# Kernel tuning notes

Measured on AMD Instinct MI355X. Metric: run time of the kernel, lower is better.

Reference implementation:

```python
import jax, jax.numpy as jnp
import numpy as np

D_IN = 1024
D_OUT = 1024
SEQ = 4096


def setup_inputs() -> dict:
    key = jax.random.key(0)
    k0, k1, k2, k3 = jax.random.split(key, 4)
    inputs = jax.random.normal(k0, (SEQ, D_IN), dtype=jnp.float32)
    # original uses torch.rand (uniform [0,1)) for weights
    W_q = jax.random.uniform(k1, (D_IN, D_OUT), dtype=jnp.float32)
    W_k = jax.random.uniform(k2, (D_IN, D_OUT), dtype=jnp.float32)
    W_v = jax.random.uniform(k3, (D_IN, D_OUT), dtype=jnp.float32)
    return {"inputs": inputs, "W_q": W_q, "W_k": W_k, "W_v": W_v}


def reference(inputs, W_q, W_k, W_v):
    queries = inputs @ W_q            # [S, d_out]
    keys = inputs @ W_k               # [S, d_out]
    values = inputs @ W_v             # [S, d_out]
    d_k = keys.shape[-1]
    scale = 1.0 / jnp.sqrt(jnp.asarray(d_k, dtype=queries.dtype))
    attn_scores = queries @ keys.T    # [S, S]
    attn_weights = jax.nn.softmax(attn_scores * scale, axis=-1)
    context_vectors = attn_weights @ values  # [S, d_out]
    return context_vectors
```

## Files before the change

kernel.cpp:

```cpp
#include <hip/hip_runtime.h>

typedef unsigned short u16;
typedef __attribute__((ext_vector_type(8))) short bf16x8;
typedef __attribute__((ext_vector_type(4))) float f32x4;

#define SEQ 4096
#define DIM 1024

__device__ __forceinline__ u16 f2bf(float f) {
  unsigned u = __float_as_uint(f);
  return (u16)((u + 0x7fffu + ((u >> 16) & 1u)) >> 16);
}
__device__ __forceinline__ float bf2f(u16 h) {
  return __uint_as_float(((unsigned)h) << 16);
}

__device__ __forceinline__ void gload_lds16(const void* g, void* l) {
  __builtin_amdgcn_global_load_lds(
      (const __attribute__((address_space(1))) void*)g,
      (__attribute__((address_space(3))) void*)l, 16, 0, 0);
}

__device__ __forceinline__ size_t pkoff(int row, int col, int kd) {
  int tile = (row >> 7) * (kd >> 5) + (col >> 5);
  int r7 = row & 127, c5 = col & 31;
  int slot = ((r7 >> 4) << 6) | ((c5 >> 3) << 4) | (r7 & 15);
  return (size_t)tile * 4096 + (size_t)(slot * 8 + (c5 & 7));
}

__device__ __forceinline__ void stage_tile_pk(const u16* __restrict__ g,
                                              u16* lds, int tid) {
  const int w = tid >> 6;
  gload_lds16(g + (size_t)tid * 8, lds + (size_t)(w * 64) * 8);
  gload_lds16(g + (size_t)(256 + tid) * 8, lds + (size_t)(256 + w * 64) * 8);
}

template <int NPAIR>
__device__ __forceinline__ void gemm_multi_pk(
    const u16* A0, const u16* A1, const u16* B0, const u16* B1,
    int nkb, u16* lds, f32x4 (&acc)[4][4]) {
  const int tid = threadIdx.x;
  const int w = tid >> 6, l = tid & 63;
  const int wm = w >> 1, wn = w & 1;
  u16* lA0 = lds;
  u16* lB0 = lds + 4096;
  u16* lA1 = lds + 8192;
  u16* lB1 = lds + 12288;

#pragma unroll
  for (int mi = 0; mi < 4; ++mi)
#pragma unroll
    for (int ni = 0; ni < 4; ++ni)
      acc[mi][ni] = (f32x4){0.f, 0.f, 0.f, 0.f};

  const int ao = wm * 2048 + l * 8;
  const int bo = wn * 2048 + l * 8;

  for (int kb = 0; kb < nkb; ++kb) {
    stage_tile_pk(A0 + (size_t)kb * 4096, lA0, tid);
    stage_tile_pk(B0 + (size_t)kb * 4096, lB0, tid);
    if constexpr (NPAIR >= 3) {
      stage_tile_pk(A1 + (size_t)kb * 4096, lA1, tid);
      stage_tile_pk(B1 + (size_t)kb * 4096, lB1, tid);
    }
    __syncthreads();
    bf16x8 a0[4], b0[4];
#pragma unroll
    for (int i = 0; i < 4; ++i) {
      a0[i] = *(const bf16x8*)(lA0 + ao + i * 512);
      b0[i] = *(const bf16x8*)(lB0 + bo + i * 512);
    }
#pragma unroll
    for (int mi = 0; mi < 4; ++mi)
#pragma unroll
      for (int ni = 0; ni < 4; ++ni)
        acc[mi][ni] = __builtin_amdgcn_mfma_f32_16x16x32_bf16(
            a0[mi], b0[ni], acc[mi][ni], 0, 0, 0);
    if constexpr (NPAIR >= 3) {
      bf16x8 b1[4];
#pragma unroll
      for (int i = 0; i < 4; ++i) b1[i] = *(const bf16x8*)(lB1 + bo + i * 512);
#pragma unroll
      for (int mi = 0; mi < 4; ++mi)
#pragma unroll
        for (int ni = 0; ni < 4; ++ni)
          acc[mi][ni] = __builtin_amdgcn_mfma_f32_16x16x32_bf16(
              a0[mi], b1[ni], acc[mi][ni], 0, 0, 0);
      bf16x8 a1[4];
#pragma unroll
      for (int i = 0; i < 4; ++i) a1[i] = *(const bf16x8*)(lA1 + ao + i * 512);
#pragma unroll
      for (int mi = 0; mi < 4; ++mi)
#pragma unroll
        for (int ni = 0; ni < 4; ++ni)
          acc[mi][ni] = __builtin_amdgcn_mfma_f32_16x16x32_bf16(
              a1[mi], b0[ni], acc[mi][ni], 0, 0, 0);
    }
    __syncthreads();
  }
}

__device__ __forceinline__ void gemm_one64(
    const u16* A, const u16* B, int nkb, u16* lds, f32x4 (&acc)[4][4]) {
  const int tid = threadIdx.x;
  const int w = tid >> 6, l = tid & 63;
  const int wm = w >> 1, wn = w & 1;
  u16* lA = lds;
  u16* lB = lds + 8192;

#pragma unroll
  for (int mi = 0; mi < 4; ++mi)
#pragma unroll
    for (int ni = 0; ni < 4; ++ni)
      acc[mi][ni] = (f32x4){0.f, 0.f, 0.f, 0.f};

  const int ao = wm * 2048 + l * 8;
  const int bo = wn * 2048 + l * 8;

  for (int kb = 0; kb < nkb; kb += 2) {
    stage_tile_pk(A + (size_t)kb * 4096, lA, tid);
    stage_tile_pk(A + (size_t)(kb + 1) * 4096, lA + 4096, tid);
    stage_tile_pk(B + (size_t)kb * 4096, lB, tid);
    stage_tile_pk(B + (size_t)(kb + 1) * 4096, lB + 4096, tid);
    __syncthreads();
#pragma unroll
    for (int h = 0; h < 2; ++h) {
      bf16x8 av[4], bv[4];
#pragma unroll
      for (int i = 0; i < 4; ++i) {
        av[i] = *(const bf16x8*)(lA + h * 4096 + ao + i * 512);
        bv[i] = *(const bf16x8*)(lB + h * 4096 + bo + i * 512);
      }
#pragma unroll
      for (int mi = 0; mi < 4; ++mi)
#pragma unroll
        for (int ni = 0; ni < 4; ++ni)
          acc[mi][ni] = __builtin_amdgcn_mfma_f32_16x16x32_bf16(
              av[mi], bv[ni], acc[mi][ni], 0, 0, 0);
    }
    __syncthreads();
  }
}

#define EPILOGUE_IDX                                          \
  const int tid = threadIdx.x, w = tid >> 6, l = tid & 63;    \
  const int wm = w >> 1, wn = w & 1, lr = l & 15, q = l >> 4; \
  (void)tid;


__global__ __launch_bounds__(256) void prep_kernel(
    const float* __restrict__ X,
    const float* __restrict__ W0, const float* __restrict__ W1, const float* __restrict__ W2,
    u16* __restrict__ Xh, u16* __restrict__ Xl,
    u16* __restrict__ H0, u16* __restrict__ L0,
    u16* __restrict__ H1, u16* __restrict__ L1,
    u16* __restrict__ H2) {
  const int z = blockIdx.z;
  const int tx = threadIdx.x, ty = threadIdx.y;
  if (z == 0) {
    int idx = (blockIdx.y * 32 + blockIdx.x) * 256 + ty * 32 + tx;
    int row = idx >> 6;
    int c0 = (idx & 63) * 16;
    u16 h[16], lo[16];
#pragma unroll
    for (int j = 0; j < 4; ++j) {
      float4 x = *(const float4*)(X + (size_t)row * DIM + c0 + j * 4);
      float v;
      v = x.x; h[j*4+0] = f2bf(v); lo[j*4+0] = f2bf(v - bf2f(h[j*4+0]));
      v = x.y; h[j*4+1] = f2bf(v); lo[j*4+1] = f2bf(v - bf2f(h[j*4+1]));
      v = x.z; h[j*4+2] = f2bf(v); lo[j*4+2] = f2bf(v - bf2f(h[j*4+2]));
      v = x.w; h[j*4+3] = f2bf(v); lo[j*4+3] = f2bf(v - bf2f(h[j*4+3]));
    }
    size_t o0 = pkoff(row, c0, DIM);
    size_t o1 = pkoff(row, c0 + 8, DIM);
#pragma unroll
    for (int j = 0; j < 2; ++j) {
      *(ushort4*)(Xh + o0 + j * 4) = *(ushort4*)(h + j * 4);
      *(ushort4*)(Xl + o0 + j * 4) = *(ushort4*)(lo + j * 4);
      *(ushort4*)(Xh + o1 + j * 4) = *(ushort4*)(h + 8 + j * 4);
      *(ushort4*)(Xl + o1 + j * 4) = *(ushort4*)(lo + 8 + j * 4);
    }
    return;
  }
  __shared__ float t[32][33];
  const float* W = (z == 1) ? W0 : (z == 2) ? W1 : W2;
  u16* H = (z == 1) ? H0 : (z == 2) ? H1 : H2;
  u16* L = (z == 1) ? L0 : (z == 2) ? L1 : nullptr;
  const int i0 = blockIdx.y * 32, o0 = blockIdx.x * 32;
#pragma unroll
  for (int m = 0; m < 4; ++m)
    t[ty + 8 * m][tx] = W[(size_t)(i0 + ty + 8 * m) * DIM + o0 + tx];
  __syncthreads();
#pragma unroll
  for (int m = 0; m < 4; ++m) {
    float v = t[tx][ty + 8 * m];
    u16 h = f2bf(v);
    size_t o = pkoff(o0 + ty + 8 * m, i0 + tx, DIM);
    H[o] = h;
    if (L) L[o] = f2bf(v - bf2f(h));
  }
}

__global__ __launch_bounds__(256) void qkv_kernel(
    const u16* __restrict__ Xh, const u16* __restrict__ Xl,
    const u16* __restrict__ Wh0, const u16* __restrict__ Wl0,
    const u16* __restrict__ Wh1, const u16* __restrict__ Wl1,
    const u16* __restrict__ Wh2,
    u16* __restrict__ Qh, u16* __restrict__ Ql,
    u16* __restrict__ Kh, u16* __restrict__ Kl,
    u16* __restrict__ VT) {
  __shared__ __align__(16) u16 lds[4 * 4096];
  const int z = blockIdx.z;
  f32x4 acc[4][4];
  if (z < 2) {
    const u16* Wh = z ? Wh1 : Wh0;
    const u16* Wl = z ? Wl1 : Wl0;
    const int row0 = blockIdx.y * 128, col0 = blockIdx.x * 128;
    gemm_multi_pk<3>(Xh + (size_t)row0 * DIM, Xl + (size_t)row0 * DIM,
                     Wh + (size_t)col0 * DIM, Wl + (size_t)col0 * DIM,
                     DIM / 32, lds, acc);
    EPILOGUE_IDX
    u16* H = z ? Kh : Qh;
    u16* L = z ? Kl : Ql;
#pragma unroll
    for (int mi = 0; mi < 4; ++mi)
#pragma unroll
      for (int ni = 0; ni < 4; ++ni)
#pragma unroll
        for (int r = 0; r < 4; ++r) {
          int row = row0 + wm * 64 + mi * 16 + q * 4 + r;
          int col = col0 + wn * 64 + ni * 16 + lr;
          float v = acc[mi][ni][r];
          u16 h = f2bf(v);
          size_t o = pkoff(row, col, DIM);
          H[o] = h;
          L[o] = f2bf(v - bf2f(h));
        }
  } else {
    const int row0 = blockIdx.x * 128;
    const int col0 = blockIdx.y * 128;
    gemm_one64(Wh2 + (size_t)row0 * DIM, Xh + (size_t)col0 * DIM,
               DIM / 32, lds, acc);
    EPILOGUE_IDX
#pragma unroll
    for (int mi = 0; mi < 4; ++mi)
#pragma unroll
      for (int ni = 0; ni < 4; ++ni)
#pragma unroll
        for (int r = 0; r < 4; ++r) {
          int row = row0 + wm * 64 + mi * 16 + q * 4 + r;
          int col = col0 + wn * 64 + ni * 16 + lr;
          VT[pkoff(row, col, SEQ)] = f2bf(acc[mi][ni][r]);
        }
  }
}

__global__ __launch_bounds__(256) void s_kernel(
    const u16* __restrict__ Qh, const u16* __restrict__ Ql,
    const u16* __restrict__ Kh, const u16* __restrict__ Kl,
    float* __restrict__ S) {
  __shared__ __align__(16) u16 lds[4 * 4096];
  const int row0 = blockIdx.y * 128, col0 = blockIdx.x * 128;
  f32x4 acc[4][4];
  gemm_multi_pk<3>(Qh + (size_t)row0 * DIM, Ql + (size_t)row0 * DIM,
                   Kh + (size_t)col0 * DIM, Kl + (size_t)col0 * DIM,
                   DIM / 32, lds, acc);
  EPILOGUE_IDX
  const float scale = 0.03125f;
#pragma unroll
  for (int mi = 0; mi < 4; ++mi)
#pragma unroll
    for (int ni = 0; ni < 4; ++ni)
#pragma unroll
      for (int r = 0; r < 4; ++r) {
        int row = row0 + wm * 64 + mi * 16 + q * 4 + r;
        int col = col0 + wn * 64 + ni * 16 + lr;
        S[(size_t)row * SEQ + col] = acc[mi][ni][r] * scale;
      }
}

__global__ __launch_bounds__(256) void softmax_kernel(const float* __restrict__ S,
                                                      u16* __restrict__ P) {
  const int row = blockIdx.x;
  const float* s = S + (size_t)row * SEQ;
  const int tid = threadIdx.x;
  float v[16];
  float mx = -3.4e38f;
#pragma unroll
  for (int i = 0; i < 16; ++i) {
    v[i] = s[tid + i * 256];
    mx = fmaxf(mx, v[i]);
  }
#pragma unroll
  for (int off = 32; off; off >>= 1) mx = fmaxf(mx, __shfl_xor(mx, off));
  __shared__ float red[8];
  const int w = tid >> 6, l = tid & 63;
  if (l == 0) red[w] = mx;
  __syncthreads();
  mx = fmaxf(fmaxf(red[0], red[1]), fmaxf(red[2], red[3]));
  float sum = 0.f;
#pragma unroll
  for (int i = 0; i < 16; ++i) {
    v[i] = __expf(v[i] - mx);
    sum += v[i];
  }
#pragma unroll
  for (int off = 32; off; off >>= 1) sum += __shfl_xor(sum, off);
  if (l == 0) red[4 + w] = sum;
  __syncthreads();
  sum = red[4] + red[5] + red[6] + red[7];
  const float inv = 1.f / sum;
#pragma unroll
  for (int i = 0; i < 16; ++i)
    P[pkoff(row, tid + i * 256, SEQ)] = f2bf(v[i] * inv);
}

__global__ __launch_bounds__(256) void o_kernel(const u16* __restrict__ P,
                                                const u16* __restrict__ VT,
                                                float* __restrict__ Opart) {
  __shared__ __align__(16) u16 lds[4 * 4096];
  const int z = blockIdx.z;
  const int row0 = blockIdx.y * 128, col0 = blockIdx.x * 128;
  const u16* A = P + (size_t)row0 * SEQ + (size_t)z * 32 * 4096;
  const u16* B = VT + (size_t)col0 * SEQ + (size_t)z * 32 * 4096;
  f32x4 acc[4][4];
  gemm_one64(A, B, 32, lds, acc);
  EPILOGUE_IDX
  float* O = Opart + (size_t)z * SEQ * DIM;
#pragma unroll
  for (int mi = 0; mi < 4; ++mi)
#pragma unroll
    for (int ni = 0; ni < 4; ++ni)
#pragma unroll
      for (int r = 0; r < 4; ++r) {
        int row = row0 + wm * 64 + mi * 16 + q * 4 + r;
        int col = col0 + wn * 64 + ni * 16 + lr;
        O[(size_t)row * DIM + col] = acc[mi][ni][r];
      }
}

__global__ __launch_bounds__(256) void o_reduce_kernel(const float* __restrict__ Op,
                                                       float* __restrict__ O) {
  const size_t N = (size_t)SEQ * DIM;
  size_t i = ((size_t)blockIdx.x * 256 + threadIdx.x) * 4;
  float4 a = *(const float4*)(Op + i);
  float4 b = *(const float4*)(Op + N + i);
  float4 c = *(const float4*)(Op + 2 * N + i);
  float4 d = *(const float4*)(Op + 3 * N + i);
  float4 r;
  r.x = (a.x + b.x) + (c.x + d.x);
  r.y = (a.y + b.y) + (c.y + d.y);
  r.z = (a.z + b.z) + (c.z + d.z);
  r.w = (a.w + b.w) + (c.w + d.w);
  *(float4*)(O + i) = r;
}

extern "C" void kernel_launch(void* const* d_in, const int* in_sizes, int n_in,
                              void* d_out, int out_size, void* d_ws, size_t ws_size,
                              hipStream_t stream) {
  const float* X = (const float*)d_in[0];
  const float* Wq = (const float*)d_in[1];
  const float* Wk = (const float*)d_in[2];
  const float* Wv = (const float*)d_in[3];

  const size_t MB = 1024 * 1024;
  char* w = (char*)d_ws;
  u16* Xh = (u16*)(w + 0 * MB);
  u16* Xl = (u16*)(w + 8 * MB);
  u16* WqhT = (u16*)(w + 16 * MB);
  u16* WqlT = (u16*)(w + 18 * MB);
  u16* WkhT = (u16*)(w + 20 * MB);
  u16* WklT = (u16*)(w + 22 * MB);
  u16* WvhT = (u16*)(w + 24 * MB);
  u16* Qh = (u16*)(w + 26 * MB);
  u16* Ql = (u16*)(w + 34 * MB);
  u16* Kh = (u16*)(w + 42 * MB);
  u16* Kl = (u16*)(w + 50 * MB);
  u16* VT = (u16*)(w + 58 * MB);
  float* S = (float*)(w + 66 * MB);
  u16* P = (u16*)(w + 26 * MB);
  float* Opart = (float*)(w + 66 * MB);

  prep_kernel<<<dim3(32, 32, 4), dim3(32, 8), 0, stream>>>(
      X, Wq, Wk, Wv, Xh, Xl, WqhT, WqlT, WkhT, WklT, WvhT);
  qkv_kernel<<<dim3(DIM / 128, SEQ / 128, 3), 256, 0, stream>>>(
      Xh, Xl, WqhT, WqlT, WkhT, WklT, WvhT, Qh, Ql, Kh, Kl, VT);
  s_kernel<<<dim3(SEQ / 128, SEQ / 128), 256, 0, stream>>>(Qh, Ql, Kh, Kl, S);
  softmax_kernel<<<SEQ, 256, 0, stream>>>(S, P);
  o_kernel<<<dim3(DIM / 128, SEQ / 128, 4), 256, 0, stream>>>(P, VT, Opart);
  o_reduce_kernel<<<(SEQ * DIM) / (256 * 4), 256, 0, stream>>>(Opart, (float*)d_out);
}
```

Measured before the change: 340.6 us.

## Switch GEMMs to 32x32x16 MFMA and vectorize prep/softmax stores

Replaces the 16x16x32 bf16 MFMA tiling (4x4 accumulators per wave) with 32x32x16 MFMA (2x2 f32x16 accumulators) in all GEMM helpers. The LDS fragment addressing and the epilogue row/column mapping are reworked for the new accumulator layout. The aim is fewer MFMA issues and fewer LDS fragment reads per K step. It also changes softmax to contiguous float4 loads and 16-byte packed stores of P, and packs the prep kernel's X stores into 16-byte writes. The risk is a wrong fragment-to-packed-layout mapping, and the epilogue's global writes become less coalesced.

```diff
diff --git a/kernel.cpp b/kernel.cpp
--- a/kernel.cpp
+++ b/kernel.cpp
@@ -2,7 +2,7 @@
 
 typedef unsigned short u16;
 typedef __attribute__((ext_vector_type(8))) short bf16x8;
-typedef __attribute__((ext_vector_type(4))) float f32x4;
+typedef __attribute__((ext_vector_type(16))) float f32x16;
 
 #define SEQ 4096
 #define DIM 1024
@@ -35,26 +35,30 @@
   gload_lds16(g + (size_t)(256 + tid) * 8, lds + (size_t)(256 + w * 64) * 8);
 }
 
+#define MFMA32(a, b, c) __builtin_amdgcn_mfma_f32_32x32x16_bf16((a), (b), (c), 0, 0, 0)
+
 template <int NPAIR>
 __device__ __forceinline__ void gemm_multi_pk(
     const u16* A0, const u16* A1, const u16* B0, const u16* B1,
-    int nkb, u16* lds, f32x4 (&acc)[4][4]) {
+    int nkb, u16* lds, f32x16 (&acc)[2][2]) {
   const int tid = threadIdx.x;
   const int w = tid >> 6, l = tid & 63;
   const int wm = w >> 1, wn = w & 1;
+  const int lbase = ((l & 31) >> 4) * 512 + (l >> 5) * 128 + (l & 15) * 8;
   u16* lA0 = lds;
   u16* lB0 = lds + 4096;
   u16* lA1 = lds + 8192;
   u16* lB1 = lds + 12288;
 
 #pragma unroll
-  for (int mi = 0; mi < 4; ++mi)
-#pragma unroll
-    for (int ni = 0; ni < 4; ++ni)
-      acc[mi][ni] = (f32x4){0.f, 0.f, 0.f, 0.f};
-
-  const int ao = wm * 2048 + l * 8;
-  const int bo = wn * 2048 + l * 8;
+  for (int ms = 0; ms < 2; ++ms)
+#pragma unroll
+    for (int ns = 0; ns < 2; ++ns)
+#pragma unroll
+      for (int i = 0; i < 16; ++i) acc[ms][ns][i] = 0.f;
+
+  const int ao = wm * 2048 + lbase;
+  const int bo = wn * 2048 + lbase;
 
   for (int kb = 0; kb < nkb; ++kb) {
     stage_tile_pk(A0 + (size_t)kb * 4096, lA0, tid);
@@ -64,58 +68,71 @@
       stage_tile_pk(B1 + (size_t)kb * 4096, lB1, tid);
     }
     __syncthreads();
-    bf16x8 a0[4], b0[4];
-#pragma unroll
-    for (int i = 0; i < 4; ++i) {
-      a0[i] = *(const bf16x8*)(lA0 + ao + i * 512);
-      b0[i] = *(const bf16x8*)(lB0 + bo + i * 512);
-    }
-#pragma unroll
-    for (int mi = 0; mi < 4; ++mi)
-#pragma unroll
-      for (int ni = 0; ni < 4; ++ni)
-        acc[mi][ni] = __builtin_amdgcn_mfma_f32_16x16x32_bf16(
-            a0[mi], b0[ni], acc[mi][ni], 0, 0, 0);
+    bf16x8 a0[2][2], b0[2][2];
+#pragma unroll
+    for (int ms = 0; ms < 2; ++ms)
+#pragma unroll
+      for (int ks = 0; ks < 2; ++ks) {
+        a0[ms][ks] = *(const bf16x8*)(lA0 + ao + ms * 1024 + ks * 256);
+        b0[ms][ks] = *(const bf16x8*)(lB0 + bo + ms * 1024 + ks * 256);
+      }
+#pragma unroll
+    for (int ms = 0; ms < 2; ++ms)
+#pragma unroll
+      for (int ns = 0; ns < 2; ++ns)
+#pragma unroll
+        for (int ks = 0; ks < 2; ++ks)
+          acc[ms][ns] = MFMA32(a0[ms][ks], b0[ns][ks], acc[ms][ns]);
     if constexpr (NPAIR >= 3) {
-      bf16x8 b1[4];
-#pragma unroll
-      for (int i = 0; i < 4; ++i) b1[i] = *(const bf16x8*)(lB1 + bo + i * 512);
-#pragma unroll
-      for (int mi = 0; mi < 4; ++mi)
-#pragma unroll
-        for (int ni = 0; ni < 4; ++ni)
-          acc[mi][ni] = __builtin_amdgcn_mfma_f32_16x16x32_bf16(
-              a0[mi], b1[ni], acc[mi][ni], 0, 0, 0);
-      bf16x8 a1[4];
-#pragma unroll
-      for (int i = 0; i < 4; ++i) a1[i] = *(const bf16x8*)(lA1 + ao + i * 512);
-#pragma unroll
-      for (int mi = 0; mi < 4; ++mi)
-#pragma unroll
-        for (int ni = 0; ni < 4; ++ni)
-          acc[mi][ni] = __builtin_amdgcn_mfma_f32_16x16x32_bf16(
-              a1[mi], b0[ni], acc[mi][ni], 0, 0, 0);
+      bf16x8 b1[2][2];
+#pragma unroll
+      for (int ns = 0; ns < 2; ++ns)
+#pragma unroll
+        for (int ks = 0; ks < 2; ++ks)
+          b1[ns][ks] = *(const bf16x8*)(lB1 + bo + ns * 1024 + ks * 256);
+#pragma unroll
+      for (int ms = 0; ms < 2; ++ms)
+#pragma unroll
+        for (int ns = 0; ns < 2; ++ns)
+#pragma unroll
+          for (int ks = 0; ks < 2; ++ks)
+            acc[ms][ns] = MFMA32(a0[ms][ks], b1[ns][ks], acc[ms][ns]);
+      bf16x8 a1[2][2];
+#pragma unroll
+      for (int ms = 0; ms < 2; ++ms)
+#pragma unroll
+        for (int ks = 0; ks < 2; ++ks)
+          a1[ms][ks] = *(const bf16x8*)(lA1 + ao + ms * 1024 + ks * 256);
+#pragma unroll
+      for (int ms = 0; ms < 2; ++ms)
+#pragma unroll
+        for (int ns = 0; ns < 2; ++ns)
+#pragma unroll
+          for (int ks = 0; ks < 2; ++ks)
+            acc[ms][ns] = MFMA32(a1[ms][ks], b0[ns][ks], acc[ms][ns]);
     }
     __syncthreads();
   }
 }
 
 __device__ __forceinline__ void gemm_one64(
-    const u16* A, const u16* B, int nkb, u16* lds, f32x4 (&acc)[4][4]) {
+    const u16* A, const u16* B, int nkb, u16* lds, f32x16 (&acc)[2][2]) {
   const int tid = threadIdx.x;
   const int w = tid >> 6, l = tid & 63;
   const int wm = w >> 1, wn = w & 1;
+  const int lbase = ((l & 31) >> 4) * 512 + (l >> 5) * 128 + (l & 15) * 8;
   u16* lA = lds;
   u16* lB = lds + 8192;
 
 #pragma unroll
-  for (int mi = 0; mi < 4; ++mi)
-#pragma unroll
-    for (int ni = 0; ni < 4; ++ni)
-      acc[mi][ni] = (f32x4){0.f, 0.f, 0.f, 0.f};
-
-  const int ao = wm * 2048 + l * 8;
-  const int bo = wn * 2048 + l * 8;
+  for (int ms = 0; ms < 2; ++ms)
+#pragma unroll
+    for (int ns = 0; ns < 2; ++ns)
+#pragma unroll
+      for (int i = 0; i < 16; ++i) acc[ms][ns][i] = 0.f;
+
+  const int ao = wm * 2048 + lbase;
+  const int bo = wn * 2048 + lbase;
 
   for (int kb = 0; kb < nkb; kb += 2) {
     stage_tile_pk(A + (size_t)kb * 4096, lA, tid);
@@ -124,28 +141,30 @@
     stage_tile_pk(B + (size_t)(kb + 1) * 4096, lB + 4096, tid);
     __syncthreads();
 #pragma unroll
-    for (int h = 0; h < 2; ++h) {
-      bf16x8 av[4], bv[4];
-#pragma unroll
-      for (int i = 0; i < 4; ++i) {
-        av[i] = *(const bf16x8*)(lA + h * 4096 + ao + i * 512);
-        bv[i] = *(const bf16x8*)(lB + h * 4096 + bo + i * 512);
-      }
-#pragma unroll
-      for (int mi = 0; mi < 4; ++mi)
-#pragma unroll
-        for (int ni = 0; ni < 4; ++ni)
-          acc[mi][ni] = __builtin_amdgcn_mfma_f32_16x16x32_bf16(
-              av[mi], bv[ni], acc[mi][ni], 0, 0, 0);
+    for (int ht = 0; ht < 2; ++ht) {
+      bf16x8 av[2][2], bv[2][2];
+#pragma unroll
+      for (int ms = 0; ms < 2; ++ms)
+#pragma unroll
+        for (int ks = 0; ks < 2; ++ks) {
+          av[ms][ks] = *(const bf16x8*)(lA + ht * 4096 + ao + ms * 1024 + ks * 256);
+          bv[ms][ks] = *(const bf16x8*)(lB + ht * 4096 + bo + ms * 1024 + ks * 256);
+        }
+#pragma unroll
+      for (int ms = 0; ms < 2; ++ms)
+#pragma unroll
+        for (int ns = 0; ns < 2; ++ns)
+#pragma unroll
+          for (int ks = 0; ks < 2; ++ks)
+            acc[ms][ns] = MFMA32(av[ms][ks], bv[ns][ks], acc[ms][ns]);
     }
     __syncthreads();
   }
 }
 
-#define EPILOGUE_IDX                                          \
-  const int tid = threadIdx.x, w = tid >> 6, l = tid & 63;    \
-  const int wm = w >> 1, wn = w & 1, lr = l & 15, q = l >> 4; \
-  (void)tid;
+#define EPILOGUE_IDX32                                     \
+  const int tid = threadIdx.x, w = tid >> 6, l = tid & 63; \
+  const int wm = w >> 1, wn = w & 1, r = l & 31, h = l >> 5; (void)tid;
 
 
 __global__ __launch_bounds__(256) void prep_kernel(
@@ -161,25 +180,27 @@
     int idx = (blockIdx.y * 32 + blockIdx.x) * 256 + ty * 32 + tx;
     int row = idx >> 6;
     int c0 = (idx & 63) * 16;
-    u16 h[16], lo[16];
+    bf16x8 h0, h1, l0v, l1v;
 #pragma unroll
     for (int j = 0; j < 4; ++j) {
       float4 x = *(const float4*)(X + (size_t)row * DIM + c0 + j * 4);
+      u16 hh, ll;
       float v;
-      v = x.x; h[j*4+0] = f2bf(v); lo[j*4+0] = f2bf(v - bf2f(h[j*4+0]));
-      v = x.y; h[j*4+1] = f2bf(v); lo[j*4+1] = f2bf(v - bf2f(h[j*4+1]));
-      v = x.z; h[j*4+2] = f2bf(v); lo[j*4+2] = f2bf(v - bf2f(h[j*4+2]));
-      v = x.w; h[j*4+3] = f2bf(v); lo[j*4+3] = f2bf(v - bf2f(h[j*4+3]));
+      v = x.x; hh = f2bf(v); ll = f2bf(v - bf2f(hh));
+      if (j < 2) { h0[j*4+0] = (short)hh; l0v[j*4+0] = (short)ll; } else { h1[(j-2)*4+0] = (short)hh; l1v[(j-2)*4+0] = (short)ll; }
+      v = x.y; hh = f2bf(v); ll = f2bf(v - bf2f(hh));
+      if (j < 2) { h0[j*4+1] = (short)hh; l0v[j*4+1] = (short)ll; } else { h1[(j-2)*4+1] = (short)hh; l1v[(j-2)*4+1] = (short)ll; }
+      v = x.z; hh = f2bf(v); ll = f2bf(v - bf2f(hh));
+      if (j < 2) { h0[j*4+2] = (short)hh; l0v[j*4+2] = (short)ll; } else { h1[(j-2)*4+2] = (short)hh; l1v[(j-2)*4+2] = (short)ll; }
+      v = x.w; hh = f2bf(v); ll = f2bf(v - bf2f(hh));
+      if (j < 2) { h0[j*4+3] = (short)hh; l0v[j*4+3] = (short)ll; } else { h1[(j-2)*4+3] = (short)hh; l1v[(j-2)*4+3] = (short)ll; }
     }
     size_t o0 = pkoff(row, c0, DIM);
     size_t o1 = pkoff(row, c0 + 8, DIM);
-#pragma unroll
-    for (int j = 0; j < 2; ++j) {
-      *(ushort4*)(Xh + o0 + j * 4) = *(ushort4*)(h + j * 4);
-      *(ushort4*)(Xl + o0 + j * 4) = *(ushort4*)(lo + j * 4);
-      *(ushort4*)(Xh + o1 + j * 4) = *(ushort4*)(h + 8 + j * 4);
-      *(ushort4*)(Xl + o1 + j * 4) = *(ushort4*)(lo + 8 + j * 4);
-    }
+    *(bf16x8*)(Xh + o0) = h0;
+    *(bf16x8*)(Xl + o0) = l0v;
+    *(bf16x8*)(Xh + o1) = h1;
+    *(bf16x8*)(Xl + o1) = l1v;
     return;
   }
   __shared__ float t[32][33];
@@ -211,7 +232,7 @@
     u16* __restrict__ VT) {
   __shared__ __align__(16) u16 lds[4 * 4096];
   const int z = blockIdx.z;
-  f32x4 acc[4][4];
+  f32x16 acc[2][2];
   if (z < 2) {
     const u16* Wh = z ? Wh1 : Wh0;
     const u16* Wl = z ? Wl1 : Wl0;
@@ -219,38 +240,38 @@
     gemm_multi_pk<3>(Xh + (size_t)row0 * DIM, Xl + (size_t)row0 * DIM,
                      Wh + (size_t)col0 * DIM, Wl + (size_t)col0 * DIM,
                      DIM / 32, lds, acc);
-    EPILOGUE_IDX
+    EPILOGUE_IDX32
     u16* H = z ? Kh : Qh;
     u16* L = z ? Kl : Ql;
 #pragma unroll
-    for (int mi = 0; mi < 4; ++mi)
-#pragma unroll
-      for (int ni = 0; ni < 4; ++ni)
-#pragma unroll
-        for (int r = 0; r < 4; ++r) {
-          int row = row0 + wm * 64 + mi * 16 + q * 4 + r;
-          int col = col0 + wn * 64 + ni * 16 + lr;
-          float v = acc[mi][ni][r];
-          u16 h = f2bf(v);
+    for (int ms = 0; ms < 2; ++ms)
+#pragma unroll
+      for (int ns = 0; ns < 2; ++ns)
+#pragma unroll
+        for (int reg = 0; reg < 16; ++reg) {
+          int row = row0 + wm * 64 + ms * 32 + (reg & 3) + 8 * (reg >> 2) + 4 * h;
+          int col = col0 + wn * 64 + ns * 32 + r;
+          float v = acc[ms][ns][reg];
+          u16 hh = f2bf(v);
           size_t o = pkoff(row, col, DIM);
-          H[o] = h;
-          L[o] = f2bf(v - bf2f(h));
+          H[o] = hh;
+          L[o] = f2bf(v - bf2f(hh));
         }
   } else {
     const int row0 = blockIdx.x * 128;
     const int col0 = blockIdx.y * 128;
     gemm_one64(Wh2 + (size_t)row0 * DIM, Xh + (size_t)col0 * DIM,
                DIM / 32, lds, acc);
-    EPILOGUE_IDX
-#pragma unroll
-    for (int mi = 0; mi < 4; ++mi)
-#pragma unroll
-      for (int ni = 0; ni < 4; ++ni)
-#pragma unroll
-        for (int r = 0; r < 4; ++r) {
-          int row = row0 + wm * 64 + mi * 16 + q * 4 + r;
-          int col = col0 + wn * 64 + ni * 16 + lr;
-          VT[pkoff(row, col, SEQ)] = f2bf(acc[mi][ni][r]);
+    EPILOGUE_IDX32
+#pragma unroll
+    for (int ms = 0; ms < 2; ++ms)
+#pragma unroll
+      for (int ns = 0; ns < 2; ++ns)
+#pragma unroll
+        for (int reg = 0; reg < 16; ++reg) {
+          int row = row0 + wm * 64 + ms * 32 + (reg & 3) + 8 * (reg >> 2) + 4 * h;
+          int col = col0 + wn * 64 + ns * 32 + r;
+          VT[pkoff(row, col, SEQ)] = f2bf(acc[ms][ns][reg]);
         }
   }
 }
@@ -261,21 +282,21 @@
     float* __restrict__ S) {
   __shared__ __align__(16) u16 lds[4 * 4096];
   const int row0 = blockIdx.y * 128, col0 = blockIdx.x * 128;
-  f32x4 acc[4][4];
+  f32x16 acc[2][2];
   gemm_multi_pk<3>(Qh + (size_t)row0 * DIM, Ql + (size_t)row0 * DIM,
                    Kh + (size_t)col0 * DIM, Kl + (size_t)col0 * DIM,
                    DIM / 32, lds, acc);
-  EPILOGUE_IDX
+  EPILOGUE_IDX32
   const float scale = 0.03125f;
 #pragma unroll
-  for (int mi = 0; mi < 4; ++mi)
-#pragma unroll
-    for (int ni = 0; ni < 4; ++ni)
-#pragma unroll
-      for (int r = 0; r < 4; ++r) {
-        int row = row0 + wm * 64 + mi * 16 + q * 4 + r;
-        int col = col0 + wn * 64 + ni * 16 + lr;
-        S[(size_t)row * SEQ + col] = acc[mi][ni][r] * scale;
+  for (int ms = 0; ms < 2; ++ms)
+#pragma unroll
+    for (int ns = 0; ns < 2; ++ns)
+#pragma unroll
+      for (int reg = 0; reg < 16; ++reg) {
+        int row = row0 + wm * 64 + ms * 32 + (reg & 3) + 8 * (reg >> 2) + 4 * h;
+        int col = col0 + wn * 64 + ns * 32 + r;
+        S[(size_t)row * SEQ + col] = acc[ms][ns][reg] * scale;
       }
 }
 
@@ -284,12 +305,14 @@
   const int row = blockIdx.x;
   const float* s = S + (size_t)row * SEQ;
   const int tid = threadIdx.x;
+  const int c0 = tid * 16;
   float v[16];
   float mx = -3.4e38f;
 #pragma unroll
-  for (int i = 0; i < 16; ++i) {
-    v[i] = s[tid + i * 256];
-    mx = fmaxf(mx, v[i]);
+  for (int j = 0; j < 4; ++j) {
+    float4 x = *(const float4*)(s + c0 + j * 4);
+    v[j * 4 + 0] = x.x; v[j * 4 + 1] = x.y; v[j * 4 + 2] = x.z; v[j * 4 + 3] = x.w;
+    mx = fmaxf(mx, fmaxf(fmaxf(x.x, x.y), fmaxf(x.z, x.w)));
   }
 #pragma unroll
   for (int off = 32; off; off >>= 1) mx = fmaxf(mx, __shfl_xor(mx, off));
@@ -310,9 +333,14 @@
   __syncthreads();
   sum = red[4] + red[5] + red[6] + red[7];
   const float inv = 1.f / sum;
-#pragma unroll
-  for (int i = 0; i < 16; ++i)
-    P[pkoff(row, tid + i * 256, SEQ)] = f2bf(v[i] * inv);
+  bf16x8 p0, p1;
+#pragma unroll
+  for (int i = 0; i < 8; ++i) {
+    p0[i] = (short)f2bf(v[i] * inv);
+    p1[i] = (short)f2bf(v[8 + i] * inv);
+  }
+  *(bf16x8*)(P + pkoff(row, c0, SEQ)) = p0;
+  *(bf16x8*)(P + pkoff(row, c0 + 8, SEQ)) = p1;
 }
 
 __global__ __launch_bounds__(256) void o_kernel(const u16* __restrict__ P,
@@ -323,19 +351,19 @@
   const int row0 = blockIdx.y * 128, col0 = blockIdx.x * 128;
   const u16* A = P + (size_t)row0 * SEQ + (size_t)z * 32 * 4096;
   const u16* B = VT + (size_t)col0 * SEQ + (size_t)z * 32 * 4096;
-  f32x4 acc[4][4];
+  f32x16 acc[2][2];
   gemm_one64(A, B, 32, lds, acc);
-  EPILOGUE_IDX
+  EPILOGUE_IDX32
   float* O = Opart + (size_t)z * SEQ * DIM;
 #pragma unroll
-  for (int mi = 0; mi < 4; ++mi)
-#pragma unroll
-    for (int ni = 0; ni < 4; ++ni)
-#pragma unroll
-      for (int r = 0; r < 4; ++r) {
-        int row = row0 + wm * 64 + mi * 16 + q * 4 + r;
-        int col = col0 + wn * 64 + ni * 16 + lr;
-        O[(size_t)row * DIM + col] = acc[mi][ni][r];
+  for (int ms = 0; ms < 2; ++ms)
+#pragma unroll
+    for (int ns = 0; ns < 2; ++ns)
+#pragma unroll
+      for (int reg = 0; reg < 16; ++reg) {
+        int row = row0 + wm * 64 + ms * 32 + (reg & 3) + 8 * (reg >> 2) + 4 * h;
+        int col = col0 + wn * 64 + ns * 32 + r;
+        O[(size_t)row * DIM + col] = acc[ms][ns][reg];
       }
 }
 
@@ -347,12 +375,12 @@
   float4 b = *(const float4*)(Op + N + i);
   float4 c = *(const float4*)(Op + 2 * N + i);
   float4 d = *(const float4*)(Op + 3 * N + i);
-  float4 r;
-  r.x = (a.x + b.x) + (c.x + d.x);
-  r.y = (a.y + b.y) + (c.y + d.y);
-  r.z = (a.z + b.z) + (c.z + d.z);
-  r.w = (a.w + b.w) + (c.w + d.w);
-  *(float4*)(O + i) = r;
+  float4 rr;
+  rr.x = (a.x + b.x) + (c.x + d.x);
+  rr.y = (a.y + b.y) + (c.y + d.y);
+  rr.z = (a.z + b.z) + (c.z + d.z);
+  rr.w = (a.w + b.w) + (c.w + d.w);
+  *(float4*)(O + i) = rr;
 }
 
 extern "C" void kernel_launch(void* const* d_in, const int* in_sizes, int n_in,
```

After: 337.8 us. About the same (-0.8%).

## Double-buffer LDS in GEMM loops and vectorize softmax and prep stores

Applied to the files above, without the earlier changes.

Both GEMM helpers now use two LDS buffers, prefetching the next k-block's tiles via global_load_lds while MFMAs run on the current one. This replaces two barriers per iteration with one and is meant to overlap global-load latency with compute. The cost is double the LDS per block (64KB), which may lower occupancy. Softmax now reads contiguous float4 spans and writes packed 16-byte bf16 stores, and the prep kernel's X conversion uses 16-byte stores instead of ushort4 pairs.

```diff
diff --git a/kernel.cpp b/kernel.cpp
--- a/kernel.cpp
+++ b/kernel.cpp
@@ -35,17 +35,12 @@
   gload_lds16(g + (size_t)(256 + tid) * 8, lds + (size_t)(256 + w * 64) * 8);
 }
 
-template <int NPAIR>
-__device__ __forceinline__ void gemm_multi_pk(
+__device__ __forceinline__ void gemm3_db(
     const u16* A0, const u16* A1, const u16* B0, const u16* B1,
     int nkb, u16* lds, f32x4 (&acc)[4][4]) {
   const int tid = threadIdx.x;
   const int w = tid >> 6, l = tid & 63;
   const int wm = w >> 1, wn = w & 1;
-  u16* lA0 = lds;
-  u16* lB0 = lds + 4096;
-  u16* lA1 = lds + 8192;
-  u16* lB1 = lds + 12288;
 
 #pragma unroll
   for (int mi = 0; mi < 4; ++mi)
@@ -56,14 +51,27 @@
   const int ao = wm * 2048 + l * 8;
   const int bo = wn * 2048 + l * 8;
 
+  stage_tile_pk(A0, lds, tid);
+  stage_tile_pk(B0, lds + 4096, tid);
+  stage_tile_pk(A1, lds + 8192, tid);
+  stage_tile_pk(B1, lds + 12288, tid);
+
   for (int kb = 0; kb < nkb; ++kb) {
-    stage_tile_pk(A0 + (size_t)kb * 4096, lA0, tid);
-    stage_tile_pk(B0 + (size_t)kb * 4096, lB0, tid);
-    if constexpr (NPAIR >= 3) {
-      stage_tile_pk(A1 + (size_t)kb * 4096, lA1, tid);
-      stage_tile_pk(B1 + (size_t)kb * 4096, lB1, tid);
+    __syncthreads();
+    if (kb + 1 < nkb) {
+      u16* nb = lds + ((kb + 1) & 1) * 16384;
+      const size_t off = (size_t)(kb + 1) * 4096;
+      stage_tile_pk(A0 + off, nb, tid);
+      stage_tile_pk(B0 + off, nb + 4096, tid);
+      stage_tile_pk(A1 + off, nb + 8192, tid);
+      stage_tile_pk(B1 + off, nb + 12288, tid);
     }
-    __syncthreads();
+    const u16* cb = lds + (kb & 1) * 16384;
+    const u16* lA0 = cb;
+    const u16* lB0 = cb + 4096;
+    const u16* lA1 = cb + 8192;
+    const u16* lB1 = cb + 12288;
+
     bf16x8 a0[4], b0[4];
 #pragma unroll
     for (int i = 0; i < 4; ++i) {
@@ -76,37 +84,33 @@
       for (int ni = 0; ni < 4; ++ni)
         acc[mi][ni] = __builtin_amdgcn_mfma_f32_16x16x32_bf16(
             a0[mi], b0[ni], acc[mi][ni], 0, 0, 0);
-    if constexpr (NPAIR >= 3) {
-      bf16x8 b1[4];
-#pragma unroll
-      for (int i = 0; i < 4; ++i) b1[i] = *(const bf16x8*)(lB1 + bo + i * 512);
-#pragma unroll
-      for (int mi = 0; mi < 4; ++mi)
-#pragma unroll
-        for (int ni = 0; ni < 4; ++ni)
-          acc[mi][ni] = __builtin_amdgcn_mfma_f32_16x16x32_bf16(
-              a0[mi], b1[ni], acc[mi][ni], 0, 0, 0);
-      bf16x8 a1[4];
-#pragma unroll
-      for (int i = 0; i < 4; ++i) a1[i] = *(const bf16x8*)(lA1 + ao + i * 512);
-#pragma unroll
-      for (int mi = 0; mi < 4; ++mi)
-#pragma unroll
-        for (int ni = 0; ni < 4; ++ni)
-          acc[mi][ni] = __builtin_amdgcn_mfma_f32_16x16x32_bf16(
-              a1[mi], b0[ni], acc[mi][ni], 0, 0, 0);
-    }
-    __syncthreads();
-  }
-}
-
-__device__ __forceinline__ void gemm_one64(
+    bf16x8 b1[4];
+#pragma unroll
+    for (int i = 0; i < 4; ++i) b1[i] = *(const bf16x8*)(lB1 + bo + i * 512);
+#pragma unroll
+    for (int mi = 0; mi < 4; ++mi)
+#pragma unroll
+      for (int ni = 0; ni < 4; ++ni)
+        acc[mi][ni] = __builtin_amdgcn_mfma_f32_16x16x32_bf16(
+            a0[mi], b1[ni], acc[mi][ni], 0, 0, 0);
+    bf16x8 a1[4];
+#pragma unroll
+    for (int i = 0; i < 4; ++i) a1[i] = *(const bf16x8*)(lA1 + ao + i * 512);
+#pragma unroll
+    for (int mi = 0; mi < 4; ++mi)
+#pragma unroll
+      for (int ni = 0; ni < 4; ++ni)
+        acc[mi][ni] = __builtin_amdgcn_mfma_f32_16x16x32_bf16(
+            a1[mi], b0[ni], acc[mi][ni], 0, 0, 0);
+  }
+  __syncthreads();
+}
+
+__device__ __forceinline__ void gemm1_db(
     const u16* A, const u16* B, int nkb, u16* lds, f32x4 (&acc)[4][4]) {
   const int tid = threadIdx.x;
   const int w = tid >> 6, l = tid & 63;
   const int wm = w >> 1, wn = w & 1;
-  u16* lA = lds;
-  u16* lB = lds + 8192;
 
 #pragma unroll
   for (int mi = 0; mi < 4; ++mi)
@@ -116,20 +120,31 @@
 
   const int ao = wm * 2048 + l * 8;
   const int bo = wn * 2048 + l * 8;
-
-  for (int kb = 0; kb < nkb; kb += 2) {
-    stage_tile_pk(A + (size_t)kb * 4096, lA, tid);
-    stage_tile_pk(A + (size_t)(kb + 1) * 4096, lA + 4096, tid);
-    stage_tile_pk(B + (size_t)kb * 4096, lB, tid);
-    stage_tile_pk(B + (size_t)(kb + 1) * 4096, lB + 4096, tid);
+  const int nit = nkb >> 1;
+
+  stage_tile_pk(A, lds, tid);
+  stage_tile_pk(A + 4096, lds + 4096, tid);
+  stage_tile_pk(B, lds + 8192, tid);
+  stage_tile_pk(B + 4096, lds + 12288, tid);
+
+  for (int it = 0; it < nit; ++it) {
     __syncthreads();
-#pragma unroll
-    for (int h = 0; h < 2; ++h) {
+    if (it + 1 < nit) {
+      u16* nb = lds + ((it + 1) & 1) * 16384;
+      const size_t off = (size_t)(it + 1) * 8192;
+      stage_tile_pk(A + off, nb, tid);
+      stage_tile_pk(A + off + 4096, nb + 4096, tid);
+      stage_tile_pk(B + off, nb + 8192, tid);
+      stage_tile_pk(B + off + 4096, nb + 12288, tid);
+    }
+    const u16* cb = lds + (it & 1) * 16384;
+#pragma unroll
+    for (int ht = 0; ht < 2; ++ht) {
       bf16x8 av[4], bv[4];
 #pragma unroll
       for (int i = 0; i < 4; ++i) {
-        av[i] = *(const bf16x8*)(lA + h * 4096 + ao + i * 512);
-        bv[i] = *(const bf16x8*)(lB + h * 4096 + bo + i * 512);
+        av[i] = *(const bf16x8*)(cb + ht * 4096 + ao + i * 512);
+        bv[i] = *(const bf16x8*)(cb + 8192 + ht * 4096 + bo + i * 512);
       }
 #pragma unroll
       for (int mi = 0; mi < 4; ++mi)
@@ -138,8 +153,8 @@
           acc[mi][ni] = __builtin_amdgcn_mfma_f32_16x16x32_bf16(
               av[mi], bv[ni], acc[mi][ni], 0, 0, 0);
     }
-    __syncthreads();
-  }
+  }
+  __syncthreads();
 }
 
 #define EPILOGUE_IDX                                          \
@@ -173,13 +188,10 @@
     }
     size_t o0 = pkoff(row, c0, DIM);
     size_t o1 = pkoff(row, c0 + 8, DIM);
-#pragma unroll
-    for (int j = 0; j < 2; ++j) {
-      *(ushort4*)(Xh + o0 + j * 4) = *(ushort4*)(h + j * 4);
-      *(ushort4*)(Xl + o0 + j * 4) = *(ushort4*)(lo + j * 4);
-      *(ushort4*)(Xh + o1 + j * 4) = *(ushort4*)(h + 8 + j * 4);
-      *(ushort4*)(Xl + o1 + j * 4) = *(ushort4*)(lo + 8 + j * 4);
-    }
+    *(bf16x8*)(Xh + o0) = *(bf16x8*)(h);
+    *(bf16x8*)(Xl + o0) = *(bf16x8*)(lo);
+    *(bf16x8*)(Xh + o1) = *(bf16x8*)(h + 8);
+    *(bf16x8*)(Xl + o1) = *(bf16x8*)(lo + 8);
     return;
   }
   __shared__ float t[32][33];
@@ -209,16 +221,16 @@
     u16* __restrict__ Qh, u16* __restrict__ Ql,
     u16* __restrict__ Kh, u16* __restrict__ Kl,
     u16* __restrict__ VT) {
-  __shared__ __align__(16) u16 lds[4 * 4096];
+  __shared__ __align__(16) u16 lds[2 * 4 * 4096];
   const int z = blockIdx.z;
   f32x4 acc[4][4];
   if (z < 2) {
     const u16* Wh = z ? Wh1 : Wh0;
     const u16* Wl = z ? Wl1 : Wl0;
     const int row0 = blockIdx.y * 128, col0 = blockIdx.x * 128;
-    gemm_multi_pk<3>(Xh + (size_t)row0 * DIM, Xl + (size_t)row0 * DIM,
-                     Wh + (size_t)col0 * DIM, Wl + (size_t)col0 * DIM,
-                     DIM / 32, lds, acc);
+    gemm3_db(Xh + (size_t)row0 * DIM, Xl + (size_t)row0 * DIM,
+             Wh + (size_t)col0 * DIM, Wl + (size_t)col0 * DIM,
+             DIM / 32, lds, acc);
     EPILOGUE_IDX
     u16* H = z ? Kh : Qh;
     u16* L = z ? Kl : Ql;
@@ -239,8 +251,8 @@
   } else {
     const int row0 = blockIdx.x * 128;
     const int col0 = blockIdx.y * 128;
-    gemm_one64(Wh2 + (size_t)row0 * DIM, Xh + (size_t)col0 * DIM,
-               DIM / 32, lds, acc);
+    gemm1_db(Wh2 + (size_t)row0 * DIM, Xh + (size_t)col0 * DIM,
+             DIM / 32, lds, acc);
     EPILOGUE_IDX
 #pragma unroll
     for (int mi = 0; mi < 4; ++mi)
@@ -259,12 +271,12 @@
     const u16* __restrict__ Qh, const u16* __restrict__ Ql,
     const u16* __restrict__ Kh, const u16* __restrict__ Kl,
     float* __restrict__ S) {
-  __shared__ __align__(16) u16 lds[4 * 4096];
+  __shared__ __align__(16) u16 lds[2 * 4 * 4096];
   const int row0 = blockIdx.y * 128, col0 = blockIdx.x * 128;
   f32x4 acc[4][4];
-  gemm_multi_pk<3>(Qh + (size_t)row0 * DIM, Ql + (size_t)row0 * DIM,
-                   Kh + (size_t)col0 * DIM, Kl + (size_t)col0 * DIM,
-                   DIM / 32, lds, acc);
+  gemm3_db(Qh + (size_t)row0 * DIM, Ql + (size_t)row0 * DIM,
+           Kh + (size_t)col0 * DIM, Kl + (size_t)col0 * DIM,
+           DIM / 32, lds, acc);
   EPILOGUE_IDX
   const float scale = 0.03125f;
 #pragma unroll
@@ -284,12 +296,14 @@
   const int row = blockIdx.x;
   const float* s = S + (size_t)row * SEQ;
   const int tid = threadIdx.x;
+  const int c0 = tid * 16;
   float v[16];
   float mx = -3.4e38f;
 #pragma unroll
-  for (int i = 0; i < 16; ++i) {
-    v[i] = s[tid + i * 256];
-    mx = fmaxf(mx, v[i]);
+  for (int j = 0; j < 4; ++j) {
+    float4 x = *(const float4*)(s + c0 + j * 4);
+    v[j * 4 + 0] = x.x; v[j * 4 + 1] = x.y; v[j * 4 + 2] = x.z; v[j * 4 + 3] = x.w;
+    mx = fmaxf(mx, fmaxf(fmaxf(x.x, x.y), fmaxf(x.z, x.w)));
   }
 #pragma unroll
   for (int off = 32; off; off >>= 1) mx = fmaxf(mx, __shfl_xor(mx, off));
@@ -310,21 +324,23 @@
   __syncthreads();
   sum = red[4] + red[5] + red[6] + red[7];
   const float inv = 1.f / sum;
-#pragma unroll
-  for (int i = 0; i < 16; ++i)
-    P[pkoff(row, tid + i * 256, SEQ)] = f2bf(v[i] * inv);
+  u16 p[16];
+#pragma unroll
+  for (int i = 0; i < 16; ++i) p[i] = f2bf(v[i] * inv);
+  *(bf16x8*)(P + pkoff(row, c0, SEQ)) = *(bf16x8*)(p);
+  *(bf16x8*)(P + pkoff(row, c0 + 8, SEQ)) = *(bf16x8*)(p + 8);
 }
 
 __global__ __launch_bounds__(256) void o_kernel(const u16* __restrict__ P,
                                                 const u16* __restrict__ VT,
                                                 float* __restrict__ Opart) {
-  __shared__ __align__(16) u16 lds[4 * 4096];
+  __shared__ __align__(16) u16 lds[2 * 4 * 4096];
   const int z = blockIdx.z;
   const int row0 = blockIdx.y * 128, col0 = blockIdx.x * 128;
   const u16* A = P + (size_t)row0 * SEQ + (size_t)z * 32 * 4096;
   const u16* B = VT + (size_t)col0 * SEQ + (size_t)z * 32 * 4096;
   f32x4 acc[4][4];
-  gemm_one64(A, B, 32, lds, acc);
+  gemm1_db(A, B, 32, lds, acc);
   EPILOGUE_IDX
   float* O = Opart + (size_t)z * SEQ * DIM;
 #pragma unroll
@@ -347,12 +363,12 @@
   float4 b = *(const float4*)(Op + N + i);
   float4 c = *(const float4*)(Op + 2 * N + i);
   float4 d = *(const float4*)(Op + 3 * N + i);
-  float4 r;
-  r.x = (a.x + b.x) + (c.x + d.x);
-  r.y = (a.y + b.y) + (c.y + d.y);
-  r.z = (a.z + b.z) + (c.z + d.z);
-  r.w = (a.w + b.w) + (c.w + d.w);
-  *(float4*)(O + i) = r;
+  float4 rr;
+  rr.x = (a.x + b.x) + (c.x + d.x);
+  rr.y = (a.y + b.y) + (c.y + d.y);
+  rr.z = (a.z + b.z) + (c.z + d.z);
+  rr.w = (a.w + b.w) + (c.w + d.w);
+  *(float4*)(O + i) = rr;
 }
 
 extern "C" void kernel_launch(void* const* d_in, const int* in_sizes, int n_in,
```

Result: faster. 317.9 us (-6.7%).
